# Kernel optimization log

Hardware: AMD Instinct MI355X
Metric: run time of the kernel (lower is better)

## Reference

```python
import jax, jax.numpy as jnp
import numpy as np

N_ROW = 50000
N_COL = 50000
E = 1_200_000
D_IN = 64
D_H = 128


def _gconv(h_src, src, dst, w_e, W, b, n_src, n_dst):
    """DGL GraphConv(norm='both') with edge weights: symmetric degree norm
    (unweighted degrees, clamped to >=1), u_mul_e message, sum reduce, then linear."""
    ones = jnp.ones_like(w_e)
    out_deg = jnp.clip(jax.ops.segment_sum(ones, src, num_segments=n_src), 1.0)
    in_deg = jnp.clip(jax.ops.segment_sum(ones, dst, num_segments=n_dst), 1.0)
    hs = h_src * jax.lax.rsqrt(out_deg)[:, None]          # [n_src, F] pre-norm
    m = hs[src] * w_e[:, None]                            # [E, F] gather + edge weight
    agg = jax.ops.segment_sum(m, dst, num_segments=n_dst)  # [n_dst, F] scatter-sum
    agg = agg * jax.lax.rsqrt(in_deg)[:, None]
    return agg @ W + b


def setup_inputs() -> dict:
    key = jax.random.key(0)
    ks = jax.random.split(key, 16)
    return {
        'feat_row': jax.random.normal(ks[0], (N_ROW, D_IN), jnp.float32),
        'feat_col': jax.random.normal(ks[1], (N_COL, D_IN), jnp.float32),
        'src_rc': jax.random.randint(ks[2], (E,), 0, N_ROW),
        'dst_rc': jax.random.randint(ks[3], (E,), 0, N_COL),
        'w_rc': jax.random.uniform(ks[4], (E,), jnp.float32),
        'src_cr': jax.random.randint(ks[5], (E,), 0, N_COL),
        'dst_cr': jax.random.randint(ks[6], (E,), 0, N_ROW),
        'w_cr': jax.random.uniform(ks[7], (E,), jnp.float32),
        'W0_rc': jax.random.normal(ks[8], (D_IN, D_H), jnp.float32) / np.float32(np.sqrt(D_IN)),
        'b0_rc': jnp.zeros((D_H,), jnp.float32),
        'W0_cr': jax.random.normal(ks[9], (D_IN, D_H), jnp.float32) / np.float32(np.sqrt(D_IN)),
        'b0_cr': jnp.zeros((D_H,), jnp.float32),
        'W1_rc': jax.random.normal(ks[10], (D_H, D_H), jnp.float32) / np.float32(np.sqrt(D_H)),
        'b1_rc': jnp.zeros((D_H,), jnp.float32),
        'W1_cr': jax.random.normal(ks[11], (D_H, D_H), jnp.float32) / np.float32(np.sqrt(D_H)),
        'b1_cr': jnp.zeros((D_H,), jnp.float32),
    }


def reference(feat_row, feat_col, src_rc, dst_rc, w_rc, src_cr, dst_cr, w_cr,
              W0_rc, b0_rc, W0_cr, b0_cr, W1_rc, b1_rc, W1_cr, b1_cr):
    # Layer 1 (HeteroGraphConv, sum across relations; each dst type has one relation) + ReLU
    h_col1 = jax.nn.relu(_gconv(feat_row, src_rc, dst_rc, w_rc, W0_rc, b0_rc, N_ROW, N_COL))
    h_row1 = jax.nn.relu(_gconv(feat_col, src_cr, dst_cr, w_cr, W0_cr, b0_cr, N_COL, N_ROW))
    # Layer 2 + ReLU
    h_col2 = jax.nn.relu(_gconv(h_row1, src_rc, dst_rc, w_rc, W1_rc, b1_rc, N_ROW, N_COL))
    h_row2 = jax.nn.relu(_gconv(h_col1, src_cr, dst_cr, w_cr, W1_cr, b1_cr, N_COL, N_ROW))
    # dgl.mean_nodes per ntype (single graph -> [1, D_H]), summed over ntypes
    hg = jnp.mean(h_row2, axis=0, keepdims=True) + jnp.mean(h_col2, axis=0, keepdims=True)
    return hg
```

## Files before the change

### kernel.cpp

```cpp
#include <hip/hip_runtime.h>
#include <stdint.h>

constexpr int NROW = 50000;
constexpr int NCOL = 50000;
constexpr int DH   = 128;
constexpr int NTAB = 200000;
constexpr int HB   = 12500;
constexpr int HBLK = 64;
constexpr int DGRID = 1250;
constexpr int GGRID = 2048;
constexpr int CH    = 500;

typedef __attribute__((ext_vector_type(8))) short short8;
typedef __attribute__((ext_vector_type(4))) float f32x4;
typedef __attribute__((ext_vector_type(2))) float f32x2;

__device__ __forceinline__ float bf_hi(unsigned u) { return __uint_as_float(u & 0xffff0000u); }
__device__ __forceinline__ unsigned short f2bf(float f) {
    unsigned u = __float_as_uint(f);
    return (unsigned short)((u + 0x7fffu + ((u >> 16) & 1u)) >> 16);
}

__device__ __forceinline__ unsigned char f2fp8(float f) {
    unsigned b = __float_as_uint(f);
    unsigned s = (b >> 24) & 0x80u;
    unsigned mag = b & 0x7fffffffu;
    if (mag >= 0x43e00000u) return (unsigned char)(s | 0x7eu);
    unsigned r = mag + 0x7ffffu + ((mag >> 20) & 1u);
    int e = (int)(r >> 23) - 120;
    if (e < 1) {
        float af = __uint_as_float(mag);
        unsigned m = (unsigned)(af * 512.f + 0.5f);
        if (m > 8u) m = 8u;
        return (unsigned char)(s | m);
    }
    return (unsigned char)(s | (unsigned)(e << 3) | ((r >> 20) & 7u));
}

#if defined(__has_builtin) && __has_builtin(__builtin_amdgcn_cvt_pk_f32_fp8)
__device__ __forceinline__ f32x2 fp8x2f(unsigned v) {
    return __builtin_amdgcn_cvt_pk_f32_fp8((int)v, false);
}
#else
__device__ __forceinline__ float fp8_1(unsigned u) {
    unsigned s = (u & 0x80u) << 24, em = u & 0x7fu;
    if (em >= 8u) return __uint_as_float(s | ((em + 960u) << 20));
    float v = (float)em * 0.001953125f;
    return (u & 0x80u) ? -v : v;
}
__device__ __forceinline__ f32x2 fp8x2f(unsigned v) {
    f32x2 r; r.x = fp8_1(v & 0xffu); r.y = fp8_1((v >> 8) & 0xffu); return r;
}
#endif

__global__ __launch_bounds__(512) void hist_lds(
        const int* __restrict__ s_rc, const int* __restrict__ d_rc,
        const int* __restrict__ s_cr, const int* __restrict__ d_cr,
        int* __restrict__ partial, int E) {
    __shared__ int h[HB];
    const int sec = blockIdx.x >> 6;
    const int blk = blockIdx.x & (HBLK - 1);
    const int tab = sec >> 2;
    const int lo  = (sec & 3) * HB;
    const int* __restrict__ arr = (tab == 0) ? s_rc : (tab == 1) ? d_rc
                                 : (tab == 2) ? s_cr : d_cr;
    for (int i = threadIdx.x; i < HB; i += blockDim.x) h[i] = 0;
    __syncthreads();
    const int stride = HBLK * blockDim.x;
    for (int i = blk * blockDim.x + threadIdx.x; i < E; i += stride) {
        int id = arr[i] - lo;
        if ((unsigned)id < (unsigned)HB) atomicAdd(&h[id], 1);
    }
    __syncthreads();
    int* __restrict__ out = partial + ((size_t)sec * HBLK + blk) * HB;
    for (int i = threadIdx.x; i < HB; i += blockDim.x) out[i] = h[i];
}

__global__ void reduce_norms2(const int* __restrict__ partial, int* __restrict__ cnt,
                              float* __restrict__ norms) {
    int stride = gridDim.x * blockDim.x;
    for (int i = blockIdx.x * blockDim.x + threadIdx.x; i < NTAB; i += stride) {
        int t = i / 50000;
        int r = i - t * 50000;
        int q = r / HB;
        int j = r - q * HB;
        const int* __restrict__ p = partial + ((size_t)(t * 4 + q) * HBLK) * HB + j;
        int s = 0;
#pragma unroll
        for (int b = 0; b < HBLK; ++b) s += p[(size_t)b * HB];
        cnt[i] = s;
        norms[i] = 1.0f / sqrtf((float)max(s, 1));
    }
}

__global__ __launch_bounds__(256) void scanA(const int* __restrict__ cnt, int* __restrict__ bsum) {
    __shared__ int red[256];
    const int c = blockIdx.x;
    const int* __restrict__ cbl = cnt + ((c >= 100) ? 150000 : 50000);
    const int j0 = (c % 100) * CH;
    int s = 0;
    for (int i = threadIdx.x; i < CH; i += 256) s += cbl[j0 + i];
    red[threadIdx.x] = s;
    __syncthreads();
    for (int off = 128; off > 0; off >>= 1) {
        if (threadIdx.x < off) red[threadIdx.x] += red[threadIdx.x + off];
        __syncthreads();
    }
    if (threadIdx.x == 0) bsum[c] = red[0];
}

__global__ void scanB(const int* __restrict__ bsum, int* __restrict__ cbase) {
    __shared__ int b[200];
    for (int i = threadIdx.x; i < 200; i += blockDim.x) b[i] = bsum[i];
    __syncthreads();
    if (threadIdx.x < 2) {
        int run = 0;
        const int o = threadIdx.x * 100;
        for (int k = 0; k < 100; ++k) { cbase[o + k] = run; run += b[o + k]; }
    }
}

__global__ __launch_bounds__(512) void scanC(const int* __restrict__ cnt,
                                             const int* __restrict__ cbase,
                                             int* __restrict__ ptr_rc, int* __restrict__ ptr_cr,
                                             int E) {
    __shared__ int buf[512];
    const int c = blockIdx.x;
    const int table = (c >= 100);
    const int* __restrict__ cbl = cnt + (table ? 150000 : 50000);
    int* __restrict__ ptr = table ? ptr_cr : ptr_rc;
    const int j0 = (c % 100) * CH;
    const int t = threadIdx.x;
    const int v = (t < CH) ? cbl[j0 + t] : 0;
    buf[t] = v;
    __syncthreads();
    for (int off = 1; off < 512; off <<= 1) {
        int tmp = (t >= off) ? buf[t - off] : 0;
        __syncthreads();
        buf[t] += tmp;
        __syncthreads();
    }
    if (t < CH) ptr[j0 + t] = cbase[c] + buf[t] - v;
    if ((c % 100) == 99 && t == 0) ptr[50000] = E;
}

__global__ void block_starts(int* __restrict__ partial,
                             const int* __restrict__ ptr_rc, const int* __restrict__ ptr_cr) {
    int stride = gridDim.x * blockDim.x;
    for (int i = blockIdx.x * blockDim.x + threadIdx.x; i < 8 * HB; i += stride) {
        int fsec = i / HB;
        int j = i - fsec * HB;
        int rel = fsec >> 2, q = fsec & 3;
        int histsec = rel * 8 + 4 + q;
        const int* __restrict__ ptr = rel ? ptr_cr : ptr_rc;
        int run = ptr[q * HB + j];
        int* __restrict__ p = partial + ((size_t)histsec * HBLK) * HB + j;
#pragma unroll
        for (int b = 0; b < HBLK; ++b) {
            int c = p[(size_t)b * HB];
            p[(size_t)b * HB] = run;
            run += c;
        }
    }
}

__global__ __launch_bounds__(512) void csr_fill_sorted(
        const int* __restrict__ sA, const int* __restrict__ dA,
        const float* __restrict__ wA, const float* __restrict__ routA, unsigned* __restrict__ pairA,
        const int* __restrict__ sB, const int* __restrict__ dB,
        const float* __restrict__ wB, const float* __restrict__ routB, unsigned* __restrict__ pairB,
        const int* __restrict__ partial, int E) {
    __shared__ int offs[HB];
    const int fsec = blockIdx.x >> 6;
    const int blk  = blockIdx.x & (HBLK - 1);
    const int rel = fsec >> 2, q = fsec & 3;
    const int histsec = rel * 8 + 4 + q;
    const int lo = q * HB;
    const int* __restrict__ src  = rel ? sB : sA;
    const int* __restrict__ dst  = rel ? dB : dA;
    const float* __restrict__ w  = rel ? wB : wA;
    const float* __restrict__ ro = rel ? routB : routA;
    unsigned* __restrict__ pair  = rel ? pairB : pairA;
    const int* __restrict__ bs = partial + ((size_t)histsec * HBLK + blk) * HB;
    for (int i = threadIdx.x; i < HB; i += blockDim.x) offs[i] = bs[i];
    __syncthreads();
    const int stride = HBLK * blockDim.x;
    for (int i = blk * blockDim.x + threadIdx.x; i < E; i += stride) {
        int id = dst[i] - lo;
        if ((unsigned)id < (unsigned)HB) {
            int pos = atomicAdd(&offs[id], 1);
            int s = src[i];
            pair[pos] = (unsigned)s | ((unsigned)f2bf(w[i] * ro[s]) << 16);
        }
    }
}

__global__ void prep_tables(const float4* __restrict__ fr, const float4* __restrict__ fc,
                            unsigned* __restrict__ f8r, unsigned* __restrict__ f8c, int nq,
                            const float* __restrict__ W0a, const float* __restrict__ W0b,
                            const float* __restrict__ W1a, const float* __restrict__ W1b,
                            unsigned short* __restrict__ wt) {
    const int total = 2 * nq + 49152;
    int stride = gridDim.x * blockDim.x;
    for (int i = blockIdx.x * blockDim.x + threadIdx.x; i < total; i += stride) {
        if (i < 2 * nq) {
            bool second = i >= nq;
            int k = second ? i - nq : i;
            float4 v = second ? fc[k] : fr[k];
            unsigned o = (unsigned)f2fp8(v.x) | ((unsigned)f2fp8(v.y) << 8)
                       | ((unsigned)f2fp8(v.z) << 16) | ((unsigned)f2fp8(v.w) << 24);
            if (second) f8c[k] = o; else f8r[k] = o;
        } else {
            int j = i - 2 * nq;
            const float* W; int K, base;
            if (j < 8192)       { W = W0a; K = 64;  base = 0; }
            else if (j < 16384) { W = W0b; K = 64;  base = 8192;  j -= 8192; }
            else if (j < 32768) { W = W1a; K = 128; base = 16384; j -= 16384; }
            else                { W = W1b; K = 128; base = 32768; j -= 32768; }
            int n = j / K, k = j - n * K;
            wt[base + n * K + k] = f2bf(W[k * DH + n]);
        }
    }
}

__global__ void gather64_2(const uint8_t* __restrict__ hA, const int* __restrict__ ptrA,
                           const unsigned* __restrict__ pairA, unsigned short* __restrict__ aggA,
                           const uint8_t* __restrict__ hB, const int* __restrict__ ptrB,
                           const unsigned* __restrict__ pairB, unsigned short* __restrict__ aggB,
                           int n) {
    const int rel  = blockIdx.x >= GGRID;
    const int bid  = rel ? blockIdx.x - GGRID : blockIdx.x;
    const uint8_t* __restrict__ h = rel ? hB : hA;
    const int* __restrict__ ptr  = rel ? ptrB : ptrA;
    const unsigned* __restrict__ pair = rel ? pairB : pairA;
    unsigned short* __restrict__ agg  = rel ? aggB : aggA;
    const int gw   = (bid * blockDim.x + threadIdx.x) >> 6;
    const int nw   = (GGRID * blockDim.x) >> 6;
    const int lane = threadIdx.x & 63;
    const int half = lane >> 5;
    const int c    = (lane & 31) << 1;
    for (int node = gw; node < n; node += nw) {
        const int beg = ptr[node], end = ptr[node + 1];
        float ax0 = 0.f, ay0 = 0.f, ax1 = 0.f, ay1 = 0.f;
        float ax2 = 0.f, ay2 = 0.f, ax3 = 0.f, ay3 = 0.f;
        int j = beg + half;
        for (; j + 6 < end; j += 8) {
            unsigned p0 = pair[j], p1 = pair[j + 2], p2 = pair[j + 4], p3 = pair[j + 6];
            unsigned h0 = *reinterpret_cast<const unsigned short*>(&h[(size_t)(p0 & 0xffffu) * 64 + c]);
            unsigned h1 = *reinterpret_cast<const unsigned short*>(&h[(size_t)(p1 & 0xffffu) * 64 + c]);
            unsigned h2 = *reinterpret_cast<const unsigned short*>(&h[(size_t)(p2 & 0xffffu) * 64 + c]);
            unsigned h3 = *reinterpret_cast<const unsigned short*>(&h[(size_t)(p3 & 0xffffu) * 64 + c]);
            f32x2 d0 = fp8x2f(h0), d1 = fp8x2f(h1), d2 = fp8x2f(h2), d3 = fp8x2f(h3);
            float w0 = bf_hi(p0), w1 = bf_hi(p1), w2 = bf_hi(p2), w3 = bf_hi(p3);
            ax0 = fmaf(d0.x, w0, ax0); ay0 = fmaf(d0.y, w0, ay0);
            ax1 = fmaf(d1.x, w1, ax1); ay1 = fmaf(d1.y, w1, ay1);
            ax2 = fmaf(d2.x, w2, ax2); ay2 = fmaf(d2.y, w2, ay2);
            ax3 = fmaf(d3.x, w3, ax3); ay3 = fmaf(d3.y, w3, ay3);
        }
        for (; j < end; j += 2) {
            unsigned p = pair[j];
            unsigned hv = *reinterpret_cast<const unsigned short*>(&h[(size_t)(p & 0xffffu) * 64 + c]);
            f32x2 d = fp8x2f(hv);
            float w = bf_hi(p);
            ax0 = fmaf(d.x, w, ax0); ay0 = fmaf(d.y, w, ay0);
        }
        float ax = (ax0 + ax1) + (ax2 + ax3);
        float ay = (ay0 + ay1) + (ay2 + ay3);
        ax += __shfl_xor(ax, 32);
        ay += __shfl_xor(ay, 32);
        if (half == 0) {
            unsigned pk = (unsigned)f2bf(ax) | ((unsigned)f2bf(ay) << 16);
            *reinterpret_cast<unsigned*>(&agg[(size_t)node * 64 + c]) = pk;
        }
    }
}

__global__ __launch_bounds__(256) void dense64_2(
        const unsigned short* __restrict__ aggA, const float* __restrict__ rinA,
        const unsigned short* __restrict__ wtA, const float* __restrict__ bA,
        unsigned short* __restrict__ outA,
        const unsigned short* __restrict__ aggB, const float* __restrict__ rinB,
        const unsigned short* __restrict__ wtB, const float* __restrict__ bB,
        unsigned short* __restrict__ outB, int n) {
    constexpr int K = 64, NCH = 2;
    const int rel = blockIdx.x >= DGRID;
    const int bid = rel ? blockIdx.x - DGRID : blockIdx.x;
    const unsigned short* __restrict__ agg = rel ? aggB : aggA;
    const float* __restrict__ rin = rel ? rinB : rinA;
    const unsigned short* __restrict__ wt = rel ? wtB : wtA;
    const float* __restrict__ b = rel ? bB : bA;
    unsigned short* __restrict__ outbf = rel ? outB : outA;

    const int wave = threadIdx.x >> 6;
    const int lane = threadIdx.x & 63;
    const int lrow = lane & 15;
    const int kgrp = lane >> 4;
    const int c0   = wave * 32;

    short8 bfr[2][NCH];
#pragma unroll
    for (int t = 0; t < 2; ++t)
#pragma unroll
        for (int ch = 0; ch < NCH; ++ch)
            bfr[t][ch] = *reinterpret_cast<const short8*>(
                &wt[(size_t)(c0 + t * 16 + lrow) * K + ch * 32 + kgrp * 8]);

    const float bias0 = b[c0 + lrow], bias1 = b[c0 + 16 + lrow];
    const int nstrip = n >> 4;
    for (int s = bid; s < nstrip; s += DGRID) {
        const int r0 = s << 4;
        f32x4 d0 = {0.f, 0.f, 0.f, 0.f}, d1 = {0.f, 0.f, 0.f, 0.f};
#pragma unroll
        for (int ch = 0; ch < NCH; ++ch) {
            short8 af = *reinterpret_cast<const short8*>(
                &agg[(size_t)(r0 + lrow) * K + ch * 32 + kgrp * 8]);
            d0 = __builtin_amdgcn_mfma_f32_16x16x32_bf16(af, bfr[0][ch], d0, 0, 0, 0);
            d1 = __builtin_amdgcn_mfma_f32_16x16x32_bf16(af, bfr[1][ch], d1, 0, 0, 0);
        }
#pragma unroll
        for (int i = 0; i < 4; ++i) {
            const int row = r0 + kgrp * 4 + i;
            const float rv = rin[row];
            outbf[(size_t)row * DH + c0 + lrow]      = f2bf(fmaxf(fmaf(rv, d0[i], bias0), 0.f));
            outbf[(size_t)row * DH + c0 + 16 + lrow] = f2bf(fmaxf(fmaf(rv, d1[i], bias1), 0.f));
        }
    }
}

__global__ __launch_bounds__(256) void h1t_gemm2(
        const unsigned short* __restrict__ hA, const unsigned short* __restrict__ wtA,
        uint8_t* __restrict__ htA,
        const unsigned short* __restrict__ hB, const unsigned short* __restrict__ wtB,
        uint8_t* __restrict__ htB, int n) {
    constexpr int K = 128, NCH = 4;
    const int rel = blockIdx.x >= DGRID;
    const int bid = rel ? blockIdx.x - DGRID : blockIdx.x;
    const unsigned short* __restrict__ h = rel ? hB : hA;
    const unsigned short* __restrict__ wt = rel ? wtB : wtA;
    uint8_t* __restrict__ ht = rel ? htB : htA;

    const int wave = threadIdx.x >> 6;
    const int lane = threadIdx.x & 63;
    const int lrow = lane & 15;
    const int kgrp = lane >> 4;
    const int c0   = wave * 32;

    short8 bfr[2][NCH];
#pragma unroll
    for (int t = 0; t < 2; ++t)
#pragma unroll
        for (int ch = 0; ch < NCH; ++ch)
            bfr[t][ch] = *reinterpret_cast<const short8*>(
                &wt[(size_t)(c0 + t * 16 + lrow) * K + ch * 32 + kgrp * 8]);

    const int nstrip = n >> 4;
    for (int s = bid; s < nstrip; s += DGRID) {
        const int r0 = s << 4;
        f32x4 d0 = {0.f, 0.f, 0.f, 0.f}, d1 = {0.f, 0.f, 0.f, 0.f};
#pragma unroll
        for (int ch = 0; ch < NCH; ++ch) {
            short8 af = *reinterpret_cast<const short8*>(
                &h[(size_t)(r0 + lrow) * K + ch * 32 + kgrp * 8]);
            d0 = __builtin_amdgcn_mfma_f32_16x16x32_bf16(af, bfr[0][ch], d0, 0, 0, 0);
            d1 = __builtin_amdgcn_mfma_f32_16x16x32_bf16(af, bfr[1][ch], d1, 0, 0, 0);
        }
#pragma unroll
        for (int i = 0; i < 4; ++i) {
            const int row = r0 + kgrp * 4 + i;
            ht[(size_t)row * DH + c0 + lrow]      = f2fp8(d0[i]);
            ht[(size_t)row * DH + c0 + 16 + lrow] = f2fp8(d1[i]);
        }
    }
}

__global__ __launch_bounds__(256) void gather_final(
        const uint8_t* __restrict__ htA, const int* __restrict__ ptrA,
        const unsigned* __restrict__ pairA, const float* __restrict__ rinA,
        const float* __restrict__ bA,
        const uint8_t* __restrict__ htB, const int* __restrict__ ptrB,
        const unsigned* __restrict__ pairB, const float* __restrict__ rinB,
        const float* __restrict__ bB,
        float* __restrict__ partsum, int n, float invn) {
    const int rel  = blockIdx.x >= GGRID;
    const int bid  = rel ? blockIdx.x - GGRID : blockIdx.x;
    const uint8_t* __restrict__ ht = rel ? htB : htA;
    const int* __restrict__ ptr  = rel ? ptrB : ptrA;
    const unsigned* __restrict__ pair = rel ? pairB : pairA;
    const float* __restrict__ rin = rel ? rinB : rinA;
    const float* __restrict__ b   = rel ? bB : bA;

    const int gw   = (bid * blockDim.x + threadIdx.x) >> 6;
    const int nw   = (GGRID * blockDim.x) >> 6;
    const int lane = threadIdx.x & 63;
    const int c    = lane << 1;
    const float bias0 = b[c], bias1 = b[c + 1];
    float m0 = 0.f, m1 = 0.f;

    for (int node = gw; node < n; node += nw) {
        const int beg = ptr[node], end = ptr[node + 1];
        float ax[8], ay[8];
#pragma unroll
        for (int u = 0; u < 8; ++u) { ax[u] = 0.f; ay[u] = 0.f; }
        int j = beg;
        for (; j + 7 < end; j += 8) {
            unsigned p[8]; unsigned hv[8];
#pragma unroll
            for (int u = 0; u < 8; ++u) p[u] = pair[j + u];
#pragma unroll
            for (int u = 0; u < 8; ++u)
                hv[u] = *reinterpret_cast<const unsigned short*>(&ht[(size_t)(p[u] & 0xffffu) * 128 + c]);
#pragma unroll
            for (int u = 0; u < 8; ++u) {
                f32x2 d = fp8x2f(hv[u]);
                float w = bf_hi(p[u]);
                ax[u] = fmaf(d.x, w, ax[u]);
                ay[u] = fmaf(d.y, w, ay[u]);
            }
        }
        for (; j < end; ++j) {
            unsigned p = pair[j];
            unsigned hv = *reinterpret_cast<const unsigned short*>(&ht[(size_t)(p & 0xffffu) * 128 + c]);
            f32x2 d = fp8x2f(hv);
            float w = bf_hi(p);
            ax[0] = fmaf(d.x, w, ax[0]); ay[0] = fmaf(d.y, w, ay[0]);
        }
        float accx = ((ax[0] + ax[1]) + (ax[2] + ax[3])) + ((ax[4] + ax[5]) + (ax[6] + ax[7]));
        float accy = ((ay[0] + ay[1]) + (ay[2] + ay[3])) + ((ay[4] + ay[5]) + (ay[6] + ay[7]));
        const float rv = rin[node];
        m0 += fmaxf(fmaf(rv, accx, bias0), 0.f);
        m1 += fmaxf(fmaf(rv, accy, bias1), 0.f);
    }

    __shared__ float red[512];
    red[threadIdx.x] = m0;
    red[256 + threadIdx.x] = m1;
    __syncthreads();
    if (threadIdx.x < 64) {
        float s0 = red[threadIdx.x] + red[threadIdx.x + 64] + red[threadIdx.x + 128] + red[threadIdx.x + 192];
        float s1 = red[256 + threadIdx.x] + red[256 + threadIdx.x + 64]
                 + red[256 + threadIdx.x + 128] + red[256 + threadIdx.x + 192];
        float* part = partsum + (size_t)blockIdx.x * DH;
        part[2 * threadIdx.x]     = s0 * invn;
        part[2 * threadIdx.x + 1] = s1 * invn;
    }
}

__global__ void reduce_out(const float* __restrict__ partial, float* __restrict__ out, int nrows) {
    const int t = threadIdx.x;
    const int per = nrows / gridDim.x;
    const int b0 = blockIdx.x * per;
    float s = 0.f;
    for (int b = b0; b < b0 + per; ++b) s += partial[(size_t)b * DH + t];
    atomicAdd(&out[t], s);
}

extern "C" void kernel_launch(void* const* d_in, const int* in_sizes, int n_in,
                              void* d_out, int out_size, void* d_ws, size_t ws_size,
                              hipStream_t stream) {
    const float* feat_row = (const float*)d_in[0];
    const float* feat_col = (const float*)d_in[1];
    const int*   src_rc   = (const int*)d_in[2];
    const int*   dst_rc   = (const int*)d_in[3];
    const float* w_rc     = (const float*)d_in[4];
    const int*   src_cr   = (const int*)d_in[5];
    const int*   dst_cr   = (const int*)d_in[6];
    const float* w_cr     = (const float*)d_in[7];
    const float* W0_rc    = (const float*)d_in[8];
    const float* b0_rc    = (const float*)d_in[9];
    const float* W0_cr    = (const float*)d_in[10];
    const float* b0_cr    = (const float*)d_in[11];
    const float* W1_rc    = (const float*)d_in[12];
    const float* b1_rc    = (const float*)d_in[13];
    const float* W1_cr    = (const float*)d_in[14];
    const float* b1_cr    = (const float*)d_in[15];
    const int E = in_sizes[2];
    float* out = (float*)d_out;

    int*   cnt     = (int*)d_ws;
    float* norms   = (float*)(cnt + 200000);
    int*   ptr_rc  = (int*)(norms + 200000);
    int*   ptr_cr  = ptr_rc + 50004;
    int*   bsum    = ptr_cr + 50004;
    int*   cbase   = bsum + 200;
    unsigned* pair_rc = (unsigned*)(cbase + 216);
    unsigned* pair_cr = pair_rc + E;
    unsigned short* agg_col = (unsigned short*)(pair_cr + E);
    unsigned short* agg_row = agg_col + (size_t)NCOL * 64;
    uint8_t* f8_row = (uint8_t*)(agg_row + (size_t)NROW * 64);
    uint8_t* f8_col = f8_row + (size_t)NROW * 64;
    unsigned short* h_col1 = (unsigned short*)(f8_col + (size_t)NCOL * 64);
    unsigned short* h_row1 = h_col1 + (size_t)NCOL * DH;
    uint8_t* ht_row = (uint8_t*)(h_row1 + (size_t)NROW * DH);
    uint8_t* ht_col = ht_row + (size_t)NROW * DH;
    float* partsum = (float*)(ht_col + (size_t)NCOL * DH);
    unsigned short* wt = (unsigned short*)(partsum + (size_t)2 * GGRID * DH);
    int* partial = (int*)agg_col;

    float* r_out_rc = norms;
    float* r_in_rc  = norms + NROW;
    float* r_out_cr = norms + NROW + NCOL;
    float* r_in_cr  = norms + NROW + 2 * NCOL;

    unsigned short* wt0_rc = wt;
    unsigned short* wt0_cr = wt + 8192;
    unsigned short* wt1_rc = wt + 16384;
    unsigned short* wt1_cr = wt + 32768;

    hist_lds<<<16 * HBLK, 512, 0, stream>>>(src_rc, dst_rc, src_cr, dst_cr, partial, E);
    reduce_norms2<<<512, 256, 0, stream>>>(partial, cnt, norms);
    scanA<<<200, 256, 0, stream>>>(cnt, bsum);
    scanB<<<1, 256, 0, stream>>>(bsum, cbase);
    scanC<<<200, 512, 0, stream>>>(cnt, cbase, ptr_rc, ptr_cr, E);
    block_starts<<<400, 256, 0, stream>>>(partial, ptr_rc, ptr_cr);
    csr_fill_sorted<<<8 * HBLK, 512, 0, stream>>>(
        src_rc, dst_rc, w_rc, r_out_rc, pair_rc,
        src_cr, dst_cr, w_cr, r_out_cr, pair_cr, partial, E);

    prep_tables<<<2048, 256, 0, stream>>>((const float4*)feat_row, (const float4*)feat_col,
                                          (unsigned*)f8_row, (unsigned*)f8_col, NROW * 64 / 4,
                                          W0_rc, W0_cr, W1_rc, W1_cr, wt);

    gather64_2<<<2 * GGRID, 256, 0, stream>>>(f8_row, ptr_rc, pair_rc, agg_col,
                                              f8_col, ptr_cr, pair_cr, agg_row, NCOL);
    dense64_2<<<2 * DGRID, 256, 0, stream>>>(agg_col, r_in_rc, wt0_rc, b0_rc, h_col1,
                                             agg_row, r_in_cr, wt0_cr, b0_cr, h_row1, NCOL);

    h1t_gemm2<<<2 * DGRID, 256, 0, stream>>>(h_row1, wt1_rc, ht_row,
                                             h_col1, wt1_cr, ht_col, NROW);
    hipMemsetAsync(out, 0, DH * sizeof(float), stream);
    gather_final<<<2 * GGRID, 256, 0, stream>>>(
        ht_row, ptr_rc, pair_rc, r_in_rc, b1_rc,
        ht_col, ptr_cr, pair_cr, r_in_cr, b1_cr,
        partsum, NCOL, 1.0f / NCOL);
    reduce_out<<<32, 128, 0, stream>>>(partsum, out, 2 * GGRID);
}
```

Measured before the change: 335.4 us.

## Store partial histograms as u16, split block starts, interleave block-to-relation mapping

The per-block histogram partials are now written as 16-bit counts instead of 32-bit ints, halving the traffic of the histogram write and of the reduce and block-start reads. Block starts go to a separate int buffer instead of being rewritten in place. The CSR fill, gather and final gather kernels now map block IDs so the two relations and the quarter sections interleave across consecutive blocks, spreading work across CUs and memory channels. u16 counts rely on no per-block bin exceeding 65535, which holds for this edge count.

New measurement: 332.9 us. About the same (-0.7%).

```diff
diff --git a/kernel.cpp b/kernel.cpp
--- a/kernel.cpp
+++ b/kernel.cpp
@@ -56,7 +56,7 @@
 __global__ __launch_bounds__(512) void hist_lds(
         const int* __restrict__ s_rc, const int* __restrict__ d_rc,
         const int* __restrict__ s_cr, const int* __restrict__ d_cr,
-        int* __restrict__ partial, int E) {
+        unsigned short* __restrict__ partial, int E) {
     __shared__ int h[HB];
     const int sec = blockIdx.x >> 6;
     const int blk = blockIdx.x & (HBLK - 1);
@@ -72,11 +72,11 @@
         if ((unsigned)id < (unsigned)HB) atomicAdd(&h[id], 1);
     }
     __syncthreads();
-    int* __restrict__ out = partial + ((size_t)sec * HBLK + blk) * HB;
-    for (int i = threadIdx.x; i < HB; i += blockDim.x) out[i] = h[i];
-}
-
-__global__ void reduce_norms2(const int* __restrict__ partial, int* __restrict__ cnt,
+    unsigned short* __restrict__ out = partial + ((size_t)sec * HBLK + blk) * HB;
+    for (int i = threadIdx.x; i < HB; i += blockDim.x) out[i] = (unsigned short)h[i];
+}
+
+__global__ void reduce_norms2(const unsigned short* __restrict__ partial, int* __restrict__ cnt,
                               float* __restrict__ norms) {
     int stride = gridDim.x * blockDim.x;
     for (int i = blockIdx.x * blockDim.x + threadIdx.x; i < NTAB; i += stride) {
@@ -84,7 +84,7 @@
         int r = i - t * 50000;
         int q = r / HB;
         int j = r - q * HB;
-        const int* __restrict__ p = partial + ((size_t)(t * 4 + q) * HBLK) * HB + j;
+        const unsigned short* __restrict__ p = partial + ((size_t)(t * 4 + q) * HBLK) * HB + j;
         int s = 0;
 #pragma unroll
         for (int b = 0; b < HBLK; ++b) s += p[(size_t)b * HB];
@@ -144,7 +144,7 @@
     if ((c % 100) == 99 && t == 0) ptr[50000] = E;
 }
 
-__global__ void block_starts(int* __restrict__ partial,
+__global__ void block_starts(const unsigned short* __restrict__ partial, int* __restrict__ bstart,
                              const int* __restrict__ ptr_rc, const int* __restrict__ ptr_cr) {
     int stride = gridDim.x * blockDim.x;
     for (int i = blockIdx.x * blockDim.x + threadIdx.x; i < 8 * HB; i += stride) {
@@ -154,12 +154,12 @@
         int histsec = rel * 8 + 4 + q;
         const int* __restrict__ ptr = rel ? ptr_cr : ptr_rc;
         int run = ptr[q * HB + j];
-        int* __restrict__ p = partial + ((size_t)histsec * HBLK) * HB + j;
+        const unsigned short* __restrict__ p = partial + ((size_t)histsec * HBLK) * HB + j;
+        int* __restrict__ o = bstart + ((size_t)fsec * HBLK) * HB + j;
 #pragma unroll
         for (int b = 0; b < HBLK; ++b) {
-            int c = p[(size_t)b * HB];
-            p[(size_t)b * HB] = run;
-            run += c;
+            o[(size_t)b * HB] = run;
+            run += p[(size_t)b * HB];
         }
     }
 }
@@ -169,19 +169,18 @@
         const float* __restrict__ wA, const float* __restrict__ routA, unsigned* __restrict__ pairA,
         const int* __restrict__ sB, const int* __restrict__ dB,
         const float* __restrict__ wB, const float* __restrict__ routB, unsigned* __restrict__ pairB,
-        const int* __restrict__ partial, int E) {
+        const int* __restrict__ bstart, int E) {
     __shared__ int offs[HB];
-    const int fsec = blockIdx.x >> 6;
-    const int blk  = blockIdx.x & (HBLK - 1);
+    const int fsec = blockIdx.x & 7;
+    const int blk  = blockIdx.x >> 3;
     const int rel = fsec >> 2, q = fsec & 3;
-    const int histsec = rel * 8 + 4 + q;
     const int lo = q * HB;
     const int* __restrict__ src  = rel ? sB : sA;
     const int* __restrict__ dst  = rel ? dB : dA;
     const float* __restrict__ w  = rel ? wB : wA;
     const float* __restrict__ ro = rel ? routB : routA;
     unsigned* __restrict__ pair  = rel ? pairB : pairA;
-    const int* __restrict__ bs = partial + ((size_t)histsec * HBLK + blk) * HB;
+    const int* __restrict__ bs = bstart + ((size_t)fsec * HBLK + blk) * HB;
     for (int i = threadIdx.x; i < HB; i += blockDim.x) offs[i] = bs[i];
     __syncthreads();
     const int stride = HBLK * blockDim.x;
@@ -228,8 +227,9 @@
                            const uint8_t* __restrict__ hB, const int* __restrict__ ptrB,
                            const unsigned* __restrict__ pairB, unsigned short* __restrict__ aggB,
                            int n) {
-    const int rel  = blockIdx.x >= GGRID;
-    const int bid  = rel ? blockIdx.x - GGRID : blockIdx.x;
+    const int low  = blockIdx.x & 7;
+    const int rel  = low >> 2;
+    const int bid  = (blockIdx.x >> 3) * 4 + (low & 3);
     const uint8_t* __restrict__ h = rel ? hB : hA;
     const int* __restrict__ ptr  = rel ? ptrB : ptrA;
     const unsigned* __restrict__ pair = rel ? pairB : pairA;
@@ -381,8 +381,9 @@
         const unsigned* __restrict__ pairB, const float* __restrict__ rinB,
         const float* __restrict__ bB,
         float* __restrict__ partsum, int n, float invn) {
-    const int rel  = blockIdx.x >= GGRID;
-    const int bid  = rel ? blockIdx.x - GGRID : blockIdx.x;
+    const int low  = blockIdx.x & 7;
+    const int rel  = low >> 2;
+    const int bid  = (blockIdx.x >> 3) * 4 + (low & 3);
     const uint8_t* __restrict__ ht = rel ? htB : htA;
     const int* __restrict__ ptr  = rel ? ptrB : ptrA;
     const unsigned* __restrict__ pair = rel ? pairB : pairA;
@@ -494,7 +495,8 @@
     uint8_t* ht_col = ht_row + (size_t)NROW * DH;
     float* partsum = (float*)(ht_col + (size_t)NCOL * DH);
     unsigned short* wt = (unsigned short*)(partsum + (size_t)2 * GGRID * DH);
-    int* partial = (int*)agg_col;
+    unsigned short* partial = (unsigned short*)agg_col;
+    int* bstart = (int*)(partial + (size_t)16 * HBLK * HB);
 
     float* r_out_rc = norms;
     float* r_in_rc  = norms + NROW;
@@ -511,10 +513,10 @@
     scanA<<<200, 256, 0, stream>>>(cnt, bsum);
     scanB<<<1, 256, 0, stream>>>(bsum, cbase);
     scanC<<<200, 512, 0, stream>>>(cnt, cbase, ptr_rc, ptr_cr, E);
-    block_starts<<<400, 256, 0, stream>>>(partial, ptr_rc, ptr_cr);
+    block_starts<<<400, 256, 0, stream>>>(partial, bstart, ptr_rc, ptr_cr);
     csr_fill_sorted<<<8 * HBLK, 512, 0, stream>>>(
         src_rc, dst_rc, w_rc, r_out_rc, pair_rc,
-        src_cr, dst_cr, w_cr, r_out_cr, pair_cr, partial, E);
+        src_cr, dst_cr, w_cr, r_out_cr, pair_cr, bstart, E);
 
     prep_tables<<<2048, 256, 0, stream>>>((const float4*)feat_row, (const float4*)feat_col,
                                           (unsigned*)f8_row, (unsigned*)f8_col, NROW * 64 / 4,
```
